# Kernel tuning notes

Hardware: AMD Instinct MI355X
Metric: run time of the kernel (lower is better)

## Reference

```python
import jax, jax.numpy as jnp
import numpy as np

GRID_SIDES = (16, 32, 64)  # levels=3, base_grid_size=16, expansion=2.0, grid_dimensions=2
BATCH, INPUT_DIM = 8192, 256


def setup_inputs() -> dict:
    key = jax.random.key(0)
    k0, k1, k2, k3 = jax.random.split(key, 4)
    x = jax.random.normal(k0, (BATCH, INPUT_DIM), dtype=jnp.float32)
    w1 = jax.random.normal(k1, (GRID_SIDES[0] ** 2, INPUT_DIM), dtype=jnp.float32)
    w2 = jax.random.normal(k2, (GRID_SIDES[1] ** 2, INPUT_DIM), dtype=jnp.float32)
    w3 = jax.random.normal(k3, (GRID_SIDES[2] ** 2, INPUT_DIM), dtype=jnp.float32)
    return {"x": x, "w1": w1, "w2": w2, "w3": w3}


def _som_level(x, w, side):
    # Squared Euclidean distances (B, N) via the expanded form; N = side*side.
    d2 = (
        jnp.sum(x * x, axis=1, keepdims=True)
        - 2.0 * (x @ w.T)
        + jnp.sum(w * w, axis=1)
    )
    bmu_flat = jnp.argmin(d2, axis=1)  # (B,)
    coords = jnp.stack(jnp.unravel_index(bmu_flat, (side, side)), axis=-1)  # (B, 2)
    # Quantization error = exact Euclidean distance to the BMU prototype.
    diff = x - w[bmu_flat]  # (B, D)
    q_err = jnp.sqrt(jnp.sum(diff * diff, axis=1))  # (B,)
    return coords, q_err


def reference(x, w1, w2, w3):
    c1, q1 = _som_level(x, w1, GRID_SIDES[0])
    c2, q2 = _som_level(x, w2, GRID_SIDES[1])
    c3, q3 = _som_level(x, w3, GRID_SIDES[2])
    return (c1, c2, c3, q1, q2, q3)
```

## Files before the change

kernel.cpp:

```cpp
#include <hip/hip_runtime.h>
#include <hip/hip_fp16.h>
#include <stdint.h>

#define DIM 256
#define KE  768

typedef _Float16 half8 __attribute__((ext_vector_type(8)));
typedef float floatx4 __attribute__((ext_vector_type(4)));

#define WS_WE_OFF    8388608
#define WS_WNORM_OFF 13893632
#define WS_XNORM_OFF 13915136
#define WS_BEST_OFF  13947904

__global__ __launch_bounds__(256) void conv_kernel(
    const float* __restrict__ x, const float* __restrict__ w1,
    const float* __restrict__ w2, const float* __restrict__ w3,
    ushort* __restrict__ Xe, ushort* __restrict__ We,
    float* __restrict__ wnorm, float* __restrict__ xnorm,
    unsigned long long* __restrict__ best) {
  if (blockIdx.x < 96) best[blockIdx.x * 256 + threadIdx.x] = ~0ull;
  int task = blockIdx.x * 4 + (threadIdx.x >> 6);
  int lane = threadIdx.x & 63;
  const float* src; ushort* dst; float* ndst;
  if (task < 8192) {
    src = x + (size_t)task * DIM; dst = Xe + (size_t)task * 512;
    ndst = xnorm + task;
  } else {
    int wi = task - 8192;
    if (wi < 256)       src = w1 + (size_t)wi * DIM;
    else if (wi < 1280) src = w2 + (size_t)(wi - 256) * DIM;
    else                src = w3 + (size_t)(wi - 1280) * DIM;
    dst = We + (size_t)wi * 512; ndst = wnorm + wi;
  }
  float4 v = *(const float4*)(src + lane * 4);
  float fv[4] = {v.x, v.y, v.z, v.w};
  float s = fv[0]*fv[0] + fv[1]*fv[1] + fv[2]*fv[2] + fv[3]*fv[3];
  #pragma unroll
  for (int o = 32; o > 0; o >>= 1) s += __shfl_xor(s, o);
  if (lane == 0) *ndst = s;

  ushort h[4], l[4];
  #pragma unroll
  for (int e = 0; e < 4; ++e) {
    __half hh = __float2half(fv[e]);
    float hf = __half2float(hh);
    __half ll = __float2half((fv[e] - hf) * 2048.0f);
    h[e] = __half_as_ushort(hh);
    l[e] = __half_as_ushort(ll);
  }
  *(ushort4*)(dst + lane * 4)       = make_ushort4(h[0], h[1], h[2], h[3]);
  *(ushort4*)(dst + 256 + lane * 4) = make_ushort4(l[0], l[1], l[2], l[3]);
}

__global__ __launch_bounds__(256) void gemm_kernel(
    const ushort* __restrict__ Xe, const ushort* __restrict__ We,
    const float* __restrict__ xnorm, const float* __restrict__ wnorm,
    unsigned long long* __restrict__ best) {
  __shared__ __align__(16) ushort As[128 * 64];
  __shared__ __align__(16) ushort Bs[128 * 64];
  unsigned long long (*red)[128] = (unsigned long long (*)[128])As;

  const int cb = blockIdx.x;
  const int r0 = blockIdx.y * 128;
  const int n0 = cb * 128;
  int level, lbase;
  if (cb < 2)       { level = 0; lbase = 0; }
  else if (cb < 10) { level = 1; lbase = 256; }
  else              { level = 2; lbase = 1280; }

  const int t = threadIdx.x;
  const int w = t >> 6;
  const int lane = t & 63;
  const int ln = lane & 15, q = lane >> 4;
  const int wm = (w >> 1) * 64, wn = (w & 1) * 64;

  floatx4 acc[4][4];
  #pragma unroll
  for (int i = 0; i < 4; ++i)
    #pragma unroll
    for (int j = 0; j < 4; ++j) acc[i][j] = (floatx4)0.0f;

  for (int k0 = 0; k0 < KE; k0 += 64) {
    if (k0 == 256) {
      #pragma unroll
      for (int i = 0; i < 4; ++i)
        #pragma unroll
        for (int j = 0; j < 4; ++j) acc[i][j] *= 2048.0f;
    }
    const int ak0 = (k0 < 512) ? (k0 & 255) : (k0 - 256);
    const int bk0 = (k0 < 512) ? k0 : (k0 - 512);
    #pragma unroll
    for (int it = 0; it < 4; ++it) {
      int p = it * 256 + t;
      int m = p >> 3;
      int c = (p & 7) ^ (m & 7);
      const ushort* ga = Xe + (size_t)(r0 + m) * 512 + ak0 + c * 8;
      const ushort* gb = We + (size_t)(n0 + m) * 512 + bk0 + c * 8;
      int lbc = it * 256 + (t & 192);
      __builtin_amdgcn_global_load_lds(
          (const __attribute__((address_space(1))) void*)ga,
          (__attribute__((address_space(3))) void*)(As + lbc * 8), 16, 0, 0);
      __builtin_amdgcn_global_load_lds(
          (const __attribute__((address_space(1))) void*)gb,
          (__attribute__((address_space(3))) void*)(Bs + lbc * 8), 16, 0, 0);
    }
    __syncthreads();
    #pragma unroll
    for (int s = 0; s < 2; ++s) {
      half8 a[4], b[4];
      #pragma unroll
      for (int mt = 0; mt < 4; ++mt) {
        int m = wm + mt * 16 + ln;
        int pos = m * 8 + ((s * 4 + q) ^ (m & 7));
        a[mt] = *(const half8*)&As[pos * 8];
      }
      #pragma unroll
      for (int nt = 0; nt < 4; ++nt) {
        int n = wn + nt * 16 + ln;
        int pos = n * 8 + ((s * 4 + q) ^ (n & 7));
        b[nt] = *(const half8*)&Bs[pos * 8];
      }
      #pragma unroll
      for (int mt = 0; mt < 4; ++mt)
        #pragma unroll
        for (int nt = 0; nt < 4; ++nt)
          acc[mt][nt] = __builtin_amdgcn_mfma_f32_16x16x32_f16(
              a[mt], b[nt], acc[mt][nt], 0, 0, 0);
    }
    __syncthreads();
  }

  float wnv[4];
  #pragma unroll
  for (int nt = 0; nt < 4; ++nt) wnv[nt] = wnorm[n0 + wn + nt * 16 + ln];

  #pragma unroll
  for (int mt = 0; mt < 4; ++mt) {
    #pragma unroll
    for (int r = 0; r < 4; ++r) {
      int rowl = wm + mt * 16 + q * 4 + r;
      float xnv = xnorm[r0 + rowl];
      unsigned long long bp = ~0ull;
      #pragma unroll
      for (int nt = 0; nt < 4; ++nt) {
        float d2 = fmaxf(xnv + wnv[nt] - acc[mt][nt][r] * 0.0009765625f, 0.0f);
        unsigned col = (unsigned)(n0 + wn + nt * 16 + ln - lbase);
        unsigned long long p =
            ((unsigned long long)__float_as_uint(d2) << 32) | col;
        bp = (p < bp) ? p : bp;
      }
      #pragma unroll
      for (int off = 1; off < 16; off <<= 1) {
        unsigned long long o = __shfl_xor(bp, off);
        bp = (o < bp) ? o : bp;
      }
      if (ln == 0) red[w & 1][rowl] = bp;
    }
  }
  __syncthreads();
  if (t < 128) {
    unsigned long long a = red[0][t], b = red[1][t];
    unsigned long long m = (a < b) ? a : b;
    atomicMin(&best[level * 8192 + r0 + t], m);
  }
}

__global__ __launch_bounds__(256) void finalize_kernel(
    const unsigned long long* __restrict__ best, float* __restrict__ out) {
  int task = blockIdx.x * 256 + threadIdx.x;
  int level = task >> 13;
  int row = task & 8191;
  unsigned side = (level == 0) ? 16u : (level == 1) ? 32u : 64u;
  unsigned long long v = best[task];
  unsigned idx = (unsigned)(v & 0xFFFFFFFFull);
  if (idx >= side * side) idx = 0;
  float d2 = __uint_as_float((unsigned)(v >> 32));
  out[level * 16384 + row * 2 + 0] = (float)(idx / side);
  out[level * 16384 + row * 2 + 1] = (float)(idx % side);
  out[49152 + level * 8192 + row] = sqrtf(d2);
}

extern "C" void kernel_launch(void* const* d_in, const int* in_sizes, int n_in,
                              void* d_out, int out_size, void* d_ws, size_t ws_size,
                              hipStream_t stream) {
  const float* x  = (const float*)d_in[0];
  const float* w1 = (const float*)d_in[1];
  const float* w2 = (const float*)d_in[2];
  const float* w3 = (const float*)d_in[3];
  ushort* Xe = (ushort*)d_ws;
  ushort* We = (ushort*)((char*)d_ws + WS_WE_OFF);
  float* wnorm = (float*)((char*)d_ws + WS_WNORM_OFF);
  float* xnorm = (float*)((char*)d_ws + WS_XNORM_OFF);
  unsigned long long* best = (unsigned long long*)((char*)d_ws + WS_BEST_OFF);

  conv_kernel<<<3392, 256, 0, stream>>>(x, w1, w2, w3, Xe, We, wnorm, xnorm,
                                        best);
  gemm_kernel<<<dim3(42, 64), 256, 0, stream>>>(Xe, We, xnorm, wnorm, best);
  finalize_kernel<<<96, 256, 0, stream>>>(best, (float*)d_out);
}
```

Baseline: 163.2 us.

## Load W fragments directly from global into registers with prefetch, drop B LDS tile

The B operand (prototype weights) is no longer staged through shared memory. Each lane now reads its MFMA fragment directly from global memory into registers, prefetching one sub-step ahead. This halves LDS usage and removes the LDS write and read traffic for B, which may allow higher occupancy. The cost is uncoalesced per-lane 16-byte global loads, with each W row re-read by the two warps that share it, and load latency that must be hidden by a single-step register prefetch.

```diff
diff --git a/kernel.cpp b/kernel.cpp
--- a/kernel.cpp
+++ b/kernel.cpp
@@ -58,7 +58,6 @@
     const float* __restrict__ xnorm, const float* __restrict__ wnorm,
     unsigned long long* __restrict__ best) {
   __shared__ __align__(16) ushort As[128 * 64];
-  __shared__ __align__(16) ushort Bs[128 * 64];
   unsigned long long (*red)[128] = (unsigned long long (*)[128])As;
 
   const int cb = blockIdx.x;
@@ -75,11 +74,21 @@
   const int ln = lane & 15, q = lane >> 4;
   const int wm = (w >> 1) * 64, wn = (w & 1) * 64;
 
+  const ushort* Wb0 = We + (size_t)(n0 + wn + ln) * 512 + q * 8;
+  const ushort* Wbn[4];
+  #pragma unroll
+  for (int nt = 0; nt < 4; ++nt) Wbn[nt] = Wb0 + nt * 16 * 512;
+
   floatx4 acc[4][4];
   #pragma unroll
   for (int i = 0; i < 4; ++i)
     #pragma unroll
     for (int j = 0; j < 4; ++j) acc[i][j] = (floatx4)0.0f;
+
+  half8 bn[4];
+  #pragma unroll
+  for (int nt = 0; nt < 4; ++nt)
+    bn[nt] = *(const half8*)(Wbn[nt]);
 
   for (int k0 = 0; k0 < KE; k0 += 64) {
     if (k0 == 256) {
@@ -89,26 +98,31 @@
         for (int j = 0; j < 4; ++j) acc[i][j] *= 2048.0f;
     }
     const int ak0 = (k0 < 512) ? (k0 & 255) : (k0 - 256);
-    const int bk0 = (k0 < 512) ? k0 : (k0 - 512);
     #pragma unroll
     for (int it = 0; it < 4; ++it) {
       int p = it * 256 + t;
       int m = p >> 3;
       int c = (p & 7) ^ (m & 7);
       const ushort* ga = Xe + (size_t)(r0 + m) * 512 + ak0 + c * 8;
-      const ushort* gb = We + (size_t)(n0 + m) * 512 + bk0 + c * 8;
       int lbc = it * 256 + (t & 192);
       __builtin_amdgcn_global_load_lds(
           (const __attribute__((address_space(1))) void*)ga,
           (__attribute__((address_space(3))) void*)(As + lbc * 8), 16, 0, 0);
-      __builtin_amdgcn_global_load_lds(
-          (const __attribute__((address_space(1))) void*)gb,
-          (__attribute__((address_space(3))) void*)(Bs + lbc * 8), 16, 0, 0);
     }
     __syncthreads();
     #pragma unroll
     for (int s = 0; s < 2; ++s) {
-      half8 a[4], b[4];
+      half8 bc[4];
+      #pragma unroll
+      for (int nt = 0; nt < 4; ++nt) bc[nt] = bn[nt];
+      {
+        const int nk0 = (s == 0) ? k0 : (k0 + 64);
+        const int nbk0 = ((nk0 < 512) ? nk0 : (nk0 - 512)) + (s ^ 1) * 32;
+        #pragma unroll
+        for (int nt = 0; nt < 4; ++nt)
+          bn[nt] = *(const half8*)(Wbn[nt] + (nk0 < KE ? nbk0 : 0));
+      }
+      half8 a[4];
       #pragma unroll
       for (int mt = 0; mt < 4; ++mt) {
         int m = wm + mt * 16 + ln;
@@ -116,17 +130,11 @@
         a[mt] = *(const half8*)&As[pos * 8];
       }
       #pragma unroll
-      for (int nt = 0; nt < 4; ++nt) {
-        int n = wn + nt * 16 + ln;
-        int pos = n * 8 + ((s * 4 + q) ^ (n & 7));
-        b[nt] = *(const half8*)&Bs[pos * 8];
-      }
-      #pragma unroll
       for (int mt = 0; mt < 4; ++mt)
         #pragma unroll
         for (int nt = 0; nt < 4; ++nt)
           acc[mt][nt] = __builtin_amdgcn_mfma_f32_16x16x32_f16(
-              a[mt], b[nt], acc[mt][nt], 0, 0, 0);
+              a[mt], bc[nt], acc[mt][nt], 0, 0, 0);
     }
     __syncthreads();
   }
```

Result: slower. 239.8 us (+46.9%).
